# Optimization experiments

Measured on AMD Instinct MI355X. Metric: run time of the kernel, lower is better.

Reference implementation:

```python
import jax, jax.numpy as jnp
import numpy as np
from jax import lax

B, H, W, C = 8, 96, 96, 256
N_HEADS = 8
HEAD_DIM = C // N_HEADS
KS = 5  # depthwise LePE kernel


def setup_inputs() -> dict:
    key = jax.random.key(0)
    ks = jax.random.split(key, 12)
    s = 0.05  # xavier-ish scale for weights
    return {
        "x": jax.random.normal(ks[0], (B, H, W, C), jnp.float32),
        "encoder_layer": jax.random.normal(ks[1], (B, H, W, C), jnp.float32),
        "Wq": jax.random.normal(ks[2], (C, C), jnp.float32) * s,
        "bq": jnp.zeros((C,), jnp.float32),
        "Wk": jax.random.normal(ks[3], (C, C), jnp.float32) * s,
        "bk": jnp.zeros((C,), jnp.float32),
        "Wv": jax.random.normal(ks[4], (C, C), jnp.float32) * s,
        "bv": jnp.zeros((C,), jnp.float32),
        "conv_w": jax.random.normal(ks[5], (KS, KS, 1, C), jnp.float32) * s,  # HWIO depthwise
        "conv_b": jnp.zeros((C,), jnp.float32),
        "Wo": jax.random.normal(ks[6], (C, C), jnp.float32) * s,
        "bo": jnp.zeros((C,), jnp.float32),
        "rel_pos": jnp.zeros((1,), jnp.int32),  # unused by the module
    }


def _dwconv(v, conv_w, conv_b):
    # depthwise 5x5, stride 1, pad 2, NHWC
    y = lax.conv_general_dilated(
        v, conv_w, window_strides=(1, 1), padding=((2, 2), (2, 2)),
        dimension_numbers=("NHWC", "HWIO", "NHWC"), feature_group_count=v.shape[-1])
    return y + conv_b


def reference(x, encoder_layer, Wq, bq, Wk, bk, Wv, bv, conv_w, conv_b, Wo, bo, rel_pos):
    b, h, w, c = x.shape
    n, d = N_HEADS, c // N_HEADS
    scaling = jnp.asarray(d, x.dtype) ** -0.5

    q = x @ Wq + bq
    k = x @ Wk + bk + encoder_layer  # embed_dim != 64 branch
    v = x @ Wv + bv + encoder_layer

    lepe = _dwconv(v, conv_w, conv_b)  # (b,h,w,c)
    k = k * scaling

    qr = q.reshape(b, h, w, n, d)
    kr = k.reshape(b, h, w, n, d)
    vr = v.reshape(b, h, w, n, d)

    # width-wise axial attention: scores (b,h,n,w,w), LOG-softmax over keys
    A_w = jax.nn.log_softmax(jnp.einsum("bhind,bhjnd->bhnij", qr, kr), axis=-1)
    v1 = jnp.einsum("bhnij,bhjnd->bhind", A_w, vr)  # (b,h,w,n,d)

    # height-wise axial attention: scores (b,w,n,h,h), LOG-softmax over keys
    A_h = jax.nn.log_softmax(jnp.einsum("biwnd,bjwnd->bwnij", qr, kr), axis=-1)
    out = jnp.einsum("bwnij,bjwnd->biwnd", A_h, v1)  # (b,h,w,n,d)

    out = out.reshape(b, h, w, c) + lepe
    return out @ Wo + bo
```

## Files before the change

kernel.cpp:

```cpp
#include <hip/hip_runtime.h>

#define B_ 8
#define S_ 96
#define C_ 256
#define NH_ 8
#define D_ 32
#define M_ (B_*S_*S_)
static const size_t SZ = (size_t)M_ * C_;

typedef unsigned short u16;
typedef short bf16x8 __attribute__((ext_vector_type(8)));
typedef _Float16 hf8 __attribute__((ext_vector_type(8)));
typedef float f32x4 __attribute__((ext_vector_type(4)));

__device__ __forceinline__ u16 f2b(float f) {
    unsigned u = __float_as_uint(f);
    return (u16)((u + 0x7FFFu + ((u >> 16) & 1u)) >> 16);
}
__device__ __forceinline__ float b2f(u16 h) { return __uint_as_float(((unsigned)h) << 16); }
__device__ __forceinline__ u16 f2h(float f) {
    _Float16 h = (_Float16)f;
    return __builtin_bit_cast(u16, h);
}

__device__ __forceinline__ void gload16(const u16* g, u16* l) {
    __builtin_amdgcn_global_load_lds(
        (const __attribute__((address_space(1))) u16*)g,
        (__attribute__((address_space(3))) u16*)l, 16, 0, 0);
}

__global__ __launch_bounds__(256) void prep_x(
    const float* __restrict__ x, u16* __restrict__ xb)
{
    size_t base = ((size_t)blockIdx.x * 256 + threadIdx.x) * 8;
    float4 a = *(const float4*)(x + base);
    float4 b = *(const float4*)(x + base + 4);
    u16 o[8] = { f2b(a.x), f2b(a.y), f2b(a.z), f2b(a.w),
                 f2b(b.x), f2b(b.y), f2b(b.z), f2b(b.w) };
    *(int4*)(xb + base) = *(int4*)o;
}

__global__ __launch_bounds__(256) void prep_w(
    const float* __restrict__ Wq, const float* __restrict__ Wk,
    const float* __restrict__ Wv, const float* __restrict__ Wo,
    u16* __restrict__ WT)
{
    int id = blockIdx.x * 256 + threadIdx.x;
    int w = id >> 16;
    int r = id & 65535;
    int n = r >> 8;
    int kk = r & 255;
    const float* Wp = (w == 0) ? Wq : (w == 1) ? Wk : (w == 2) ? Wv : Wo;
    WT[(size_t)id] = f2b(Wp[(size_t)kk * 256 + n]);
}

__global__ __launch_bounds__(256) void prep_cw(
    const float* __restrict__ cw, u16* __restrict__ cwh)
{
    int id = blockIdx.x * 256 + threadIdx.x;
    cwh[id] = f2h(cw[id]);
}

#define STG(lds, gbase, k0)                                                     \
    _Pragma("unroll")                                                           \
    for (int i_ = 0; i_ < 2; ++i_) {                                            \
        int r16 = wave * 32 + i_ * 16;                                          \
        gload16((gbase) + (size_t)(r16 + srow) * C_ + (k0) + sslot * 8,         \
                (lds) + r16 * 32);                                              \
    }
#define FRAG(lds, cur, rowi) \
    (*(const bf16x8*)((lds) + (cur) * 4096 + (rowi) * 32 + (kg ^ (((rowi) >> 1) & 3)) * 8))

__global__ __launch_bounds__(256, 3) void proj_q(
    const u16* __restrict__ xb, const u16* __restrict__ WT,
    const float* __restrict__ bq, u16* __restrict__ q)
{
    __shared__ u16 sA[3 * 4096];
    __shared__ u16 sB[3 * 4096];
    const int t = threadIdx.x;
    const int colbase = blockIdx.x * 128;
    const int m0 = blockIdx.y * 128;
    const int wave = t >> 6, lane = t & 63;
    const int wr = wave >> 1, wc = wave & 1;
    const int l16 = lane & 15, kg = lane >> 4;
    const int srow = lane >> 2;
    const int sslot = (lane & 3) ^ ((lane >> 3) & 3);

    const u16* gA = xb + (size_t)m0 * C_;
    const u16* gB = WT + (size_t)colbase * C_;

    f32x4 acc[4][4];
#pragma unroll
    for (int i = 0; i < 4; ++i)
#pragma unroll
        for (int j = 0; j < 4; ++j) acc[i][j] = (f32x4){0.f, 0.f, 0.f, 0.f};

    STG(sA, gA, 0); STG(sB, gB, 0);
    STG(sA + 4096, gA, 32); STG(sB + 4096, gB, 32);
#pragma unroll
    for (int it = 0; it < 8; ++it) {
        const int cur = it % 3;
        if (it < 7) asm volatile("s_waitcnt vmcnt(4)" ::: "memory");
        else        asm volatile("s_waitcnt vmcnt(0)" ::: "memory");
        __builtin_amdgcn_s_barrier();
        __builtin_amdgcn_sched_barrier(0);
        if (it < 6) { STG(sA + ((it + 2) % 3) * 4096, gA, (it + 2) * 32);
                      STG(sB + ((it + 2) % 3) * 4096, gB, (it + 2) * 32); }
        bf16x8 af[4], bf[4];
#pragma unroll
        for (int mi = 0; mi < 4; ++mi)
            af[mi] = FRAG(sA, cur, wr * 64 + mi * 16 + l16);
#pragma unroll
        for (int ni = 0; ni < 4; ++ni)
            bf[ni] = FRAG(sB, cur, wc * 64 + ni * 16 + l16);
#pragma unroll
        for (int mi = 0; mi < 4; ++mi)
#pragma unroll
            for (int ni = 0; ni < 4; ++ni)
                acc[mi][ni] = __builtin_amdgcn_mfma_f32_16x16x32_bf16(
                    af[mi], bf[ni], acc[mi][ni], 0, 0, 0);
    }

#pragma unroll
    for (int mi = 0; mi < 4; ++mi)
#pragma unroll
        for (int ni = 0; ni < 4; ++ni) {
            int col = colbase + wc * 64 + ni * 16 + l16;
            float bqv = bq[col];
#pragma unroll
            for (int r = 0; r < 4; ++r) {
                int row = m0 + wr * 64 + mi * 16 + kg * 4 + r;
                q[(size_t)row * 256 + col] = f2b(acc[mi][ni][r] + bqv);
            }
        }
}

__global__ __launch_bounds__(256, 2) void proj_kv(
    const u16* __restrict__ xb, const float* __restrict__ enc,
    const u16* __restrict__ WT,
    const float* __restrict__ bk, const float* __restrict__ bv,
    u16* __restrict__ k, u16* __restrict__ v)
{
    __shared__ u16 sA[3 * 4096];
    __shared__ u16 sB0[3 * 4096];
    __shared__ u16 sB1[3 * 4096];
    const int t = threadIdx.x;
    const int colbase = blockIdx.x * 128;
    const int m0 = blockIdx.y * 128;
    const int wave = t >> 6, lane = t & 63;
    const int wr = wave >> 1, wc = wave & 1;
    const int l16 = lane & 15, kg = lane >> 4;
    const int srow = lane >> 2;
    const int sslot = (lane & 3) ^ ((lane >> 3) & 3);

    const u16* gA = xb + (size_t)m0 * C_;
    const u16* gB0 = WT + 65536 + (size_t)colbase * C_;
    const u16* gB1 = WT + 2 * 65536 + (size_t)colbase * C_;

    f32x4 acck[4][4], accv[4][4];
#pragma unroll
    for (int i = 0; i < 4; ++i)
#pragma unroll
        for (int j = 0; j < 4; ++j) {
            acck[i][j] = (f32x4){0.f, 0.f, 0.f, 0.f};
            accv[i][j] = (f32x4){0.f, 0.f, 0.f, 0.f};
        }

    STG(sA, gA, 0); STG(sB0, gB0, 0); STG(sB1, gB1, 0);
    STG(sA + 4096, gA, 32); STG(sB0 + 4096, gB0, 32); STG(sB1 + 4096, gB1, 32);
#pragma unroll
    for (int it = 0; it < 8; ++it) {
        const int cur = it % 3;
        if (it < 7) asm volatile("s_waitcnt vmcnt(6)" ::: "memory");
        else        asm volatile("s_waitcnt vmcnt(0)" ::: "memory");
        __builtin_amdgcn_s_barrier();
        __builtin_amdgcn_sched_barrier(0);
        if (it < 6) {
            int nb = ((it + 2) % 3) * 4096;
            STG(sA + nb, gA, (it + 2) * 32);
            STG(sB0 + nb, gB0, (it + 2) * 32);
            STG(sB1 + nb, gB1, (it + 2) * 32);
        }
        bf16x8 af[4], b0[4], b1[4];
#pragma unroll
        for (int mi = 0; mi < 4; ++mi)
            af[mi] = FRAG(sA, cur, wr * 64 + mi * 16 + l16);
#pragma unroll
        for (int ni = 0; ni < 4; ++ni) {
            b0[ni] = FRAG(sB0, cur, wc * 64 + ni * 16 + l16);
            b1[ni] = FRAG(sB1, cur, wc * 64 + ni * 16 + l16);
        }
#pragma unroll
        for (int mi = 0; mi < 4; ++mi)
#pragma unroll
            for (int ni = 0; ni < 4; ++ni) {
                acck[mi][ni] = __builtin_amdgcn_mfma_f32_16x16x32_bf16(
                    af[mi], b0[ni], acck[mi][ni], 0, 0, 0);
                accv[mi][ni] = __builtin_amdgcn_mfma_f32_16x16x32_bf16(
                    af[mi], b1[ni], accv[mi][ni], 0, 0, 0);
            }
    }

    const float SCALE = 0.17677669529663687f;
#pragma unroll
    for (int mi = 0; mi < 4; ++mi)
#pragma unroll
        for (int ni = 0; ni < 4; ++ni) {
            int col = colbase + wc * 64 + ni * 16 + l16;
            float bkv = bk[col], bvv = bv[col];
#pragma unroll
            for (int r = 0; r < 4; ++r) {
                int row = m0 + wr * 64 + mi * 16 + kg * 4 + r;
                size_t off = (size_t)row * 256 + col;
                float e = enc[off];
                k[off] = f2b((acck[mi][ni][r] + bkv + e) * SCALE);
                v[off] = f2h(accv[mi][ni][r] + bvv + e);
            }
        }
}

__global__ __launch_bounds__(256) void dwconv5x5(
    const u16* __restrict__ vh, const u16* __restrict__ cwh,
    const float* __restrict__ cb, u16* __restrict__ lepeb)
{
    size_t tid = (size_t)blockIdx.x * 256 + threadIdx.x;
    int c8 = (int)(tid & 31);
    size_t rest = tid >> 5;
    int wi = (int)(rest % 12);
    size_t tmp = rest / 12;
    int h = (int)(tmp % S_);
    int b = (int)(tmp / S_);
    int w0 = wi * 8;
    int c0 = c8 * 8;

    hf8 z;
#pragma unroll
    for (int q = 0; q < 8; ++q) z[q] = (_Float16)0.f;
    hf8 acc[8] = { z, z, z, z, z, z, z, z };

#pragma unroll
    for (int dy = -2; dy <= 2; ++dy) {
        int hy = h + dy;
        if (hy < 0 || hy >= S_) continue;
        const u16* rowp = vh + (((size_t)b * S_ + hy) * S_) * C_ + c0;
        hf8 vr[12];
#pragma unroll
        for (int i = 0; i < 12; ++i) {
            int c = w0 - 2 + i;
            vr[i] = (c >= 0 && c < S_) ? *(const hf8*)(rowp + (size_t)c * C_) : z;
        }
#pragma unroll
        for (int dx = 0; dx < 5; ++dx) {
            hf8 ww = *(const hf8*)(cwh + (size_t)((dy + 2) * 5 + dx) * C_ + c0);
#pragma unroll
            for (int r = 0; r < 8; ++r) acc[r] += vr[dx + r] * ww;
        }
    }

    float4 cb0 = *(const float4*)(cb + c0);
    float4 cb1 = *(const float4*)(cb + c0 + 4);
    float cbv[8] = { cb0.x, cb0.y, cb0.z, cb0.w, cb1.x, cb1.y, cb1.z, cb1.w };
    size_t pix0 = ((size_t)b * S_ + h) * S_ + w0;
#pragma unroll
    for (int r = 0; r < 8; ++r) {
        u16 o[8];
#pragma unroll
        for (int q = 0; q < 8; ++q) o[q] = f2b((float)acc[r][q] + cbv[q]);
        *(int4*)(lepeb + (pix0 + r) * C_ + c0) = *(int4*)o;
    }
}

template<int HM>
__global__ __launch_bounds__(128, 3) void axial(
    const u16* __restrict__ qb, const u16* __restrict__ kb,
    const void* __restrict__ vin, void* __restrict__ vout,
    const u16* __restrict__ lep, int ofac, int pstride)
{
    __shared__ u16 sQ[96][56];
    __shared__ u16 sK[96][56];
    __shared__ u16 sVT[HM + 1][32][104];
    __shared__ u16 sAh[2][16][40];
    __shared__ u16 sAl[2][16][40];

    const int t = threadIdx.x;
    const int wave = t >> 6, lane = t & 63;
    const int l16 = lane & 15, kg = lane >> 4;

    const int n = blockIdx.x & 7;
    const int o = (blockIdx.x >> 3) % 96;
    const int b = blockIdx.x / (8 * 96);
    const size_t base = ((size_t)b * 9216 + (size_t)o * ofac) * C_ + n * D_;

    if (t < 96) {
        const u16* gq = qb + base + (size_t)t * pstride;
        const u16* gk = kb + base + (size_t)t * pstride;
#pragma unroll
        for (int c = 0; c < 4; ++c) {
            *(int4*)&sQ[t][c * 8] = *(const int4*)(gq + c * 8);
            *(int4*)&sK[t][c * 8] = *(const int4*)(gk + c * 8);
        }
    }
    if (HM == 0) {
        const u16* vb = (const u16*)vin;
#pragma unroll
        for (int p = 0; p < 3; ++p) {
            int j = p * 32 + (t >> 2);
            int dc = (t & 3) * 8;
            int4 raw = *(const int4*)(vb + base + (size_t)j * pstride + dc);
            const u16* e = (const u16*)&raw;
#pragma unroll
            for (int q = 0; q < 8; ++q) sVT[0][dc + q][j] = e[q];
        }
    } else {
        const float* v1 = (const float*)vin;
#pragma unroll
        for (int p = 0; p < 6; ++p) {
            int j = p * 16 + (t >> 3);
            int db = (t & 7) * 4;
            float4 f = *(const float4*)(v1 + base + (size_t)j * pstride + db);
            float fv[4] = { f.x, f.y, f.z, f.w };
#pragma unroll
            for (int q = 0; q < 4; ++q) {
                u16 hi = f2b(fv[q]);
                sVT[0][db + q][j] = hi;
                sVT[HM][db + q][j] = f2b(fv[q] - b2f(hi));
            }
        }
    }
    __syncthreads();

    bf16x8 kf[6];
#pragma unroll
    for (int f = 0; f < 6; ++f)
        kf[f] = *(const bf16x8*)&sK[f * 16 + l16][kg * 8];

    const f32x4 zero = {0.f, 0.f, 0.f, 0.f};

    for (int p = 0; p < 3; ++p) {
        const int g = wave * 3 + p;
        bf16x8 qf = *(const bf16x8*)&sQ[g * 16 + l16][kg * 8];
        f32x4 s[6];
#pragma unroll
        for (int f = 0; f < 6; ++f)
            s[f] = __builtin_amdgcn_mfma_f32_16x16x32_bf16(kf[f], qf, zero, 0, 0, 0);

        float m = s[0][0];
#pragma unroll
        for (int f = 0; f < 6; ++f)
#pragma unroll
            for (int r = 0; r < 4; ++r) m = fmaxf(m, s[f][r]);
        m = fmaxf(m, __shfl_xor(m, 16));
        m = fmaxf(m, __shfl_xor(m, 32));
        float l = 0.f;
#pragma unroll
        for (int f = 0; f < 6; ++f)
#pragma unroll
            for (int r = 0; r < 4; ++r) l += __expf(s[f][r] - m);
        l += __shfl_xor(l, 16);
        l += __shfl_xor(l, 32);
        float lse = m + __logf(l);

        u16 ah[6][4], al[6][4];
#pragma unroll
        for (int f = 0; f < 6; ++f)
#pragma unroll
            for (int r = 0; r < 4; ++r) {
                float a = s[f][r] - lse;
                ah[f][r] = (HM == 0) ? f2h(a) : f2b(a);
                if (HM) al[f][r] = f2b(a - b2f(ah[f][r]));
            }

        f32x4 pacc[2] = { zero, zero };
#pragma unroll
        for (int c = 0; c < 3; ++c) {
#pragma unroll
            for (int fi = 0; fi < 2; ++fi)
#pragma unroll
                for (int r = 0; r < 4; ++r) {
                    int col = fi * 16 + kg * 4 + r;
                    sAh[wave][l16][col] = ah[2 * c + fi][r];
                    if (HM) sAl[wave][l16][col] = al[2 * c + fi][r];
                }
            if (HM == 0) {
                hf8 ahf = *(const hf8*)&sAh[wave][l16][kg * 8];
#pragma unroll
                for (int nf = 0; nf < 2; ++nf) {
                    hf8 vt = *(const hf8*)&sVT[0][nf * 16 + l16][c * 32 + kg * 8];
                    pacc[nf] = __builtin_amdgcn_mfma_f32_16x16x32_f16(ahf, vt, pacc[nf], 0, 0, 0);
                }
            } else {
                bf16x8 ahf = *(const bf16x8*)&sAh[wave][l16][kg * 8];
                bf16x8 alf = *(const bf16x8*)&sAl[wave][l16][kg * 8];
#pragma unroll
                for (int nf = 0; nf < 2; ++nf) {
                    bf16x8 vt = *(const bf16x8*)&sVT[0][nf * 16 + l16][c * 32 + kg * 8];
                    bf16x8 vtl = *(const bf16x8*)&sVT[HM][nf * 16 + l16][c * 32 + kg * 8];
                    pacc[nf] = __builtin_amdgcn_mfma_f32_16x16x32_bf16(ahf, vt, pacc[nf], 0, 0, 0);
                    pacc[nf] = __builtin_amdgcn_mfma_f32_16x16x32_bf16(ahf, vtl, pacc[nf], 0, 0, 0);
                    pacc[nf] = __builtin_amdgcn_mfma_f32_16x16x32_bf16(alf, vt, pacc[nf], 0, 0, 0);
                }
            }
        }

#pragma unroll
        for (int nf = 0; nf < 2; ++nf)
#pragma unroll
            for (int r = 0; r < 4; ++r) {
                int qi = g * 16 + kg * 4 + r;
                size_t off = base + (size_t)qi * pstride + nf * 16 + l16;
                if (HM == 0) {
                    ((float*)vout)[off] = pacc[nf][r];
                } else {
                    float lv = b2f(lep[off]);
                    ((u16*)vout)[off] = f2b(pacc[nf][r] + lv);
                }
            }
    }
}

__global__ __launch_bounds__(256, 3) void out_gemm(
    const u16* __restrict__ o2b, const u16* __restrict__ WoT,
    const float* __restrict__ bo, float* __restrict__ out)
{
    __shared__ u16 sA[3 * 4096];
    __shared__ u16 sB[3 * 4096];
    const int t = threadIdx.x;
    const int colbase = blockIdx.x * 128;
    const int m0 = blockIdx.y * 128;
    const int wave = t >> 6, lane = t & 63;
    const int wr = wave >> 1, wc = wave & 1;
    const int l16 = lane & 15, kg = lane >> 4;
    const int srow = lane >> 2;
    const int sslot = (lane & 3) ^ ((lane >> 3) & 3);

    const u16* gA = o2b + (size_t)m0 * C_;
    const u16* gB = WoT + (size_t)colbase * C_;

    f32x4 acc[4][4];
#pragma unroll
    for (int i = 0; i < 4; ++i)
#pragma unroll
        for (int j = 0; j < 4; ++j) acc[i][j] = (f32x4){0.f, 0.f, 0.f, 0.f};

    STG(sA, gA, 0); STG(sB, gB, 0);
    STG(sA + 4096, gA, 32); STG(sB + 4096, gB, 32);
#pragma unroll
    for (int it = 0; it < 8; ++it) {
        const int cur = it % 3;
        if (it < 7) asm volatile("s_waitcnt vmcnt(4)" ::: "memory");
        else        asm volatile("s_waitcnt vmcnt(0)" ::: "memory");
        __builtin_amdgcn_s_barrier();
        __builtin_amdgcn_sched_barrier(0);
        if (it < 6) { STG(sA + ((it + 2) % 3) * 4096, gA, (it + 2) * 32);
                      STG(sB + ((it + 2) % 3) * 4096, gB, (it + 2) * 32); }
        bf16x8 af[4], bf[4];
#pragma unroll
        for (int mi = 0; mi < 4; ++mi)
            af[mi] = FRAG(sA, cur, wr * 64 + mi * 16 + l16);
#pragma unroll
        for (int ni = 0; ni < 4; ++ni)
            bf[ni] = FRAG(sB, cur, wc * 64 + ni * 16 + l16);
#pragma unroll
        for (int mi = 0; mi < 4; ++mi)
#pragma unroll
            for (int ni = 0; ni < 4; ++ni)
                acc[mi][ni] = __builtin_amdgcn_mfma_f32_16x16x32_bf16(
                    af[mi], bf[ni], acc[mi][ni], 0, 0, 0);
    }

#pragma unroll
    for (int mi = 0; mi < 4; ++mi)
#pragma unroll
        for (int ni = 0; ni < 4; ++ni) {
            int col = colbase + wc * 64 + ni * 16 + l16;
            float bv_ = bo[col];
#pragma unroll
            for (int r = 0; r < 4; ++r) {
                int row = m0 + wr * 64 + mi * 16 + kg * 4 + r;
                out[(size_t)row * 256 + col] = acc[mi][ni][r] + bv_;
            }
        }
}

extern "C" void kernel_launch(void* const* d_in, const int* in_sizes, int n_in,
                              void* d_out, int out_size, void* d_ws, size_t ws_size,
                              hipStream_t stream)
{
    const float* x   = (const float*)d_in[0];
    const float* enc = (const float*)d_in[1];
    const float* Wq  = (const float*)d_in[2];
    const float* bq  = (const float*)d_in[3];
    const float* Wk  = (const float*)d_in[4];
    const float* bk  = (const float*)d_in[5];
    const float* Wv  = (const float*)d_in[6];
    const float* bv  = (const float*)d_in[7];
    const float* cw  = (const float*)d_in[8];
    const float* cb  = (const float*)d_in[9];
    const float* Wo  = (const float*)d_in[10];
    const float* bo  = (const float*)d_in[11];

    u16* qbuf = (u16*)d_ws;
    u16* kbuf = qbuf + SZ;
    u16* vbuf = kbuf + SZ;
    u16* WT   = vbuf + SZ;
    u16* cwh  = WT + 4 * 65536;
    u16* xb   = cwh + 6400;
    u16* lep  = xb + SZ;
    float* v1 = (float*)d_out;

    prep_x<<<9216, 256, 0, stream>>>(x, xb);
    prep_w<<<1024, 256, 0, stream>>>(Wq, Wk, Wv, Wo, WT);
    prep_cw<<<25, 256, 0, stream>>>(cw, cwh);
    proj_q<<<dim3(2, 576), 256, 0, stream>>>(xb, WT, bq, qbuf);
    proj_kv<<<dim3(2, 576), 256, 0, stream>>>(xb, enc, WT, bk, bv, kbuf, vbuf);
    dwconv5x5<<<1152, 256, 0, stream>>>(vbuf, cwh, cb, lep);
    axial<0><<<B_ * 96 * NH_, 128, 0, stream>>>(qbuf, kbuf, vbuf, v1, nullptr, 96, 256);
    axial<1><<<B_ * 96 * NH_, 128, 0, stream>>>(qbuf, kbuf, v1, qbuf, lep, 1, 96 * 256);
    out_gemm<<<dim3(2, 576), 256, 0, stream>>>(qbuf, WT + 3 * 65536, bo, (float*)d_out);
}
```

Measured before the change: 291.5 us.

## Stage GEMM epilogues through LDS for vector stores; store v1 as fp16

The three GEMM kernels now transpose their accumulators through a swizzled shared-memory buffer, one half-tile at a time. Each thread then writes contiguous 16-byte vectors of q/k/v/out, with bias and encoder loads vectorised as well; previously each thread issued scattered 2- or 4-byte stores. Separately, the intermediate v1 between the two axial passes is stored as fp16 instead of fp32, and the second pass uses a single fp16 MFMA instead of the three-product bf16 hi/lo split. This cuts intermediate traffic and matrix work but lowers the precision of the height-wise attention, since log-softmax values can be large in magnitude.

```diff
diff --git a/kernel.cpp b/kernel.cpp
--- a/kernel.cpp
+++ b/kernel.cpp
@@ -71,12 +71,27 @@
 #define FRAG(lds, cur, rowi) \
     (*(const bf16x8*)((lds) + (cur) * 4096 + (rowi) * 32 + (kg ^ (((rowi) >> 1) & 3)) * 8))
 
+#define TPUT(sT, accs)                                                          \
+    _Pragma("unroll")                                                           \
+    for (int mi = 0; mi < 4; ++mi)                                              \
+    _Pragma("unroll")                                                           \
+        for (int ni = 0; ni < 4; ++ni) {                                        \
+            int colq = wc * 16 + ni * 4 + (l16 >> 2);                           \
+            _Pragma("unroll")                                                   \
+            for (int r = 0; r < 4; ++r) {                                       \
+                int row = mi * 16 + kg * 4 + r;                                 \
+                (sT)[row * 128 + ((colq ^ (row & 31)) << 2) + (l16 & 3)] =      \
+                    accs[mi][ni][r];                                            \
+            }                                                                   \
+        }
+
 __global__ __launch_bounds__(256, 3) void proj_q(
     const u16* __restrict__ xb, const u16* __restrict__ WT,
     const float* __restrict__ bq, u16* __restrict__ q)
 {
-    __shared__ u16 sA[3 * 4096];
-    __shared__ u16 sB[3 * 4096];
+    __shared__ u16 smem[24576];
+    u16* sA = smem;
+    u16* sB = smem + 12288;
     const int t = threadIdx.x;
     const int colbase = blockIdx.x * 128;
     const int m0 = blockIdx.y * 128;
@@ -121,18 +136,30 @@
                     af[mi], bf[ni], acc[mi][ni], 0, 0, 0);
     }
 
-#pragma unroll
-    for (int mi = 0; mi < 4; ++mi)
-#pragma unroll
-        for (int ni = 0; ni < 4; ++ni) {
-            int col = colbase + wc * 64 + ni * 16 + l16;
-            float bqv = bq[col];
-#pragma unroll
-            for (int r = 0; r < 4; ++r) {
-                int row = m0 + wr * 64 + mi * 16 + kg * 4 + r;
-                q[(size_t)row * 256 + col] = f2b(acc[mi][ni][r] + bqv);
-            }
-        }
+    float* sT = (float*)smem;
+    const int erow = t >> 2, cg = t & 3;
+    __syncthreads();
+#pragma unroll
+    for (int half = 0; half < 2; ++half) {
+        if (half) __syncthreads();
+        if (wr == half) { TPUT(sT, acc); }
+        __syncthreads();
+        int grow = m0 + half * 64 + erow;
+        u16 outv[32];
+#pragma unroll
+        for (int i = 0; i < 8; ++i) {
+            int cql = cg * 8 + i;
+            float4 vv = *(float4*)&sT[erow * 128 + ((cql ^ (erow & 31)) << 2)];
+            float4 bb = *(const float4*)(bq + colbase + cql * 4);
+            outv[i * 4 + 0] = f2b(vv.x + bb.x);
+            outv[i * 4 + 1] = f2b(vv.y + bb.y);
+            outv[i * 4 + 2] = f2b(vv.z + bb.z);
+            outv[i * 4 + 3] = f2b(vv.w + bb.w);
+        }
+        u16* dst = q + (size_t)grow * 256 + colbase + cg * 32;
+#pragma unroll
+        for (int s = 0; s < 4; ++s) *(int4*)(dst + s * 8) = *(int4*)(outv + s * 8);
+    }
 }
 
 __global__ __launch_bounds__(256, 2) void proj_kv(
@@ -141,9 +168,10 @@
     const float* __restrict__ bk, const float* __restrict__ bv,
     u16* __restrict__ k, u16* __restrict__ v)
 {
-    __shared__ u16 sA[3 * 4096];
-    __shared__ u16 sB0[3 * 4096];
-    __shared__ u16 sB1[3 * 4096];
+    __shared__ u16 smem[36864];
+    u16* sA  = smem;
+    u16* sB0 = smem + 12288;
+    u16* sB1 = smem + 24576;
     const int t = threadIdx.x;
     const int colbase = blockIdx.x * 128;
     const int m0 = blockIdx.y * 128;
@@ -202,21 +230,44 @@
     }
 
     const float SCALE = 0.17677669529663687f;
-#pragma unroll
-    for (int mi = 0; mi < 4; ++mi)
-#pragma unroll
-        for (int ni = 0; ni < 4; ++ni) {
-            int col = colbase + wc * 64 + ni * 16 + l16;
-            float bkv = bk[col], bvv = bv[col];
-#pragma unroll
-            for (int r = 0; r < 4; ++r) {
-                int row = m0 + wr * 64 + mi * 16 + kg * 4 + r;
-                size_t off = (size_t)row * 256 + col;
-                float e = enc[off];
-                k[off] = f2b((acck[mi][ni][r] + bkv + e) * SCALE);
-                v[off] = f2h(accv[mi][ni][r] + bvv + e);
-            }
-        }
+    float* sTk = (float*)smem;
+    float* sTv = (float*)smem + 8192;
+    const int erow = t >> 2, cg = t & 3;
+    __syncthreads();
+#pragma unroll
+    for (int half = 0; half < 2; ++half) {
+        if (half) __syncthreads();
+        if (wr == half) { TPUT(sTk, acck); TPUT(sTv, accv); }
+        __syncthreads();
+        int grow = m0 + half * 64 + erow;
+        const float* ep = enc + (size_t)grow * 256 + colbase + cg * 32;
+        u16 ko[32], vo[32];
+#pragma unroll
+        for (int i = 0; i < 8; ++i) {
+            int cql = cg * 8 + i;
+            int soff = erow * 128 + ((cql ^ (erow & 31)) << 2);
+            float4 kv = *(float4*)&sTk[soff];
+            float4 vv = *(float4*)&sTv[soff];
+            float4 ee = *(const float4*)(ep + i * 4);
+            float4 kb = *(const float4*)(bk + colbase + cql * 4);
+            float4 vb_ = *(const float4*)(bv + colbase + cql * 4);
+            ko[i * 4 + 0] = f2b((kv.x + kb.x + ee.x) * SCALE);
+            ko[i * 4 + 1] = f2b((kv.y + kb.y + ee.y) * SCALE);
+            ko[i * 4 + 2] = f2b((kv.z + kb.z + ee.z) * SCALE);
+            ko[i * 4 + 3] = f2b((kv.w + kb.w + ee.w) * SCALE);
+            vo[i * 4 + 0] = f2h(vv.x + vb_.x + ee.x);
+            vo[i * 4 + 1] = f2h(vv.y + vb_.y + ee.y);
+            vo[i * 4 + 2] = f2h(vv.z + vb_.z + ee.z);
+            vo[i * 4 + 3] = f2h(vv.w + vb_.w + ee.w);
+        }
+        u16* kd = k + (size_t)grow * 256 + colbase + cg * 32;
+        u16* vd = v + (size_t)grow * 256 + colbase + cg * 32;
+#pragma unroll
+        for (int s = 0; s < 4; ++s) {
+            *(int4*)(kd + s * 8) = *(int4*)(ko + s * 8);
+            *(int4*)(vd + s * 8) = *(int4*)(vo + s * 8);
+        }
+    }
 }
 
 __global__ __launch_bounds__(256) void dwconv5x5(
@@ -273,14 +324,13 @@
 template<int HM>
 __global__ __launch_bounds__(128, 3) void axial(
     const u16* __restrict__ qb, const u16* __restrict__ kb,
-    const void* __restrict__ vin, void* __restrict__ vout,
+    const u16* __restrict__ vin, void* __restrict__ vout,
     const u16* __restrict__ lep, int ofac, int pstride)
 {
     __shared__ u16 sQ[96][56];
     __shared__ u16 sK[96][56];
-    __shared__ u16 sVT[HM + 1][32][104];
+    __shared__ u16 sVT[32][104];
     __shared__ u16 sAh[2][16][40];
-    __shared__ u16 sAl[2][16][40];
 
     const int t = threadIdx.x;
     const int wave = t >> 6, lane = t & 63;
@@ -300,32 +350,14 @@
             *(int4*)&sK[t][c * 8] = *(const int4*)(gk + c * 8);
         }
     }
-    if (HM == 0) {
-        const u16* vb = (const u16*)vin;
-#pragma unroll
-        for (int p = 0; p < 3; ++p) {
-            int j = p * 32 + (t >> 2);
-            int dc = (t & 3) * 8;
-            int4 raw = *(const int4*)(vb + base + (size_t)j * pstride + dc);
-            const u16* e = (const u16*)&raw;
-#pragma unroll
-            for (int q = 0; q < 8; ++q) sVT[0][dc + q][j] = e[q];
-        }
-    } else {
-        const float* v1 = (const float*)vin;
-#pragma unroll
-        for (int p = 0; p < 6; ++p) {
-            int j = p * 16 + (t >> 3);
-            int db = (t & 7) * 4;
-            float4 f = *(const float4*)(v1 + base + (size_t)j * pstride + db);
-            float fv[4] = { f.x, f.y, f.z, f.w };
-#pragma unroll
-            for (int q = 0; q < 4; ++q) {
-                u16 hi = f2b(fv[q]);
-                sVT[0][db + q][j] = hi;
-                sVT[HM][db + q][j] = f2b(fv[q] - b2f(hi));
-            }
-        }
+#pragma unroll
+    for (int p = 0; p < 3; ++p) {
+        int j = p * 32 + (t >> 2);
+        int dc = (t & 3) * 8;
+        int4 raw = *(const int4*)(vin + base + (size_t)j * pstride + dc);
+        const u16* e = (const u16*)&raw;
+#pragma unroll
+        for (int q = 0; q < 8; ++q) sVT[dc + q][j] = e[q];
     }
     __syncthreads();
 
@@ -360,15 +392,12 @@
         l += __shfl_xor(l, 32);
         float lse = m + __logf(l);
 
-        u16 ah[6][4], al[6][4];
+        u16 ah[6][4];
 #pragma unroll
         for (int f = 0; f < 6; ++f)
 #pragma unroll
-            for (int r = 0; r < 4; ++r) {
-                float a = s[f][r] - lse;
-                ah[f][r] = (HM == 0) ? f2h(a) : f2b(a);
-                if (HM) al[f][r] = f2b(a - b2f(ah[f][r]));
-            }
+            for (int r = 0; r < 4; ++r)
+                ah[f][r] = f2h(s[f][r] - lse);
 
         f32x4 pacc[2] = { zero, zero };
 #pragma unroll
@@ -376,29 +405,13 @@
 #pragma unroll
             for (int fi = 0; fi < 2; ++fi)
 #pragma unroll
-                for (int r = 0; r < 4; ++r) {
-                    int col = fi * 16 + kg * 4 + r;
-                    sAh[wave][l16][col] = ah[2 * c + fi][r];
-                    if (HM) sAl[wave][l16][col] = al[2 * c + fi][r];
-                }
-            if (HM == 0) {
-                hf8 ahf = *(const hf8*)&sAh[wave][l16][kg * 8];
-#pragma unroll
-                for (int nf = 0; nf < 2; ++nf) {
-                    hf8 vt = *(const hf8*)&sVT[0][nf * 16 + l16][c * 32 + kg * 8];
-                    pacc[nf] = __builtin_amdgcn_mfma_f32_16x16x32_f16(ahf, vt, pacc[nf], 0, 0, 0);
-                }
-            } else {
-                bf16x8 ahf = *(const bf16x8*)&sAh[wave][l16][kg * 8];
-                bf16x8 alf = *(const bf16x8*)&sAl[wave][l16][kg * 8];
-#pragma unroll
-                for (int nf = 0; nf < 2; ++nf) {
-                    bf16x8 vt = *(const bf16x8*)&sVT[0][nf * 16 + l16][c * 32 + kg * 8];
-                    bf16x8 vtl = *(const bf16x8*)&sVT[HM][nf * 16 + l16][c * 32 + kg * 8];
-                    pacc[nf] = __builtin_amdgcn_mfma_f32_16x16x32_bf16(ahf, vt, pacc[nf], 0, 0, 0);
-                    pacc[nf] = __builtin_amdgcn_mfma_f32_16x16x32_bf16(ahf, vtl, pacc[nf], 0, 0, 0);
-                    pacc[nf] = __builtin_amdgcn_mfma_f32_16x16x32_bf16(alf, vt, pacc[nf], 0, 0, 0);
-                }
+                for (int r = 0; r < 4; ++r)
+                    sAh[wave][l16][fi * 16 + kg * 4 + r] = ah[2 * c + fi][r];
+            hf8 ahf = *(const hf8*)&sAh[wave][l16][kg * 8];
+#pragma unroll
+            for (int nf = 0; nf < 2; ++nf) {
+                hf8 vt = *(const hf8*)&sVT[nf * 16 + l16][c * 32 + kg * 8];
+                pacc[nf] = __builtin_amdgcn_mfma_f32_16x16x32_f16(ahf, vt, pacc[nf], 0, 0, 0);
             }
         }
 
@@ -409,7 +422,7 @@
                 int qi = g * 16 + kg * 4 + r;
                 size_t off = base + (size_t)qi * pstride + nf * 16 + l16;
                 if (HM == 0) {
-                    ((float*)vout)[off] = pacc[nf][r];
+                    ((u16*)vout)[off] = f2h(pacc[nf][r]);
                 } else {
                     float lv = b2f(lep[off]);
                     ((u16*)vout)[off] = f2b(pacc[nf][r] + lv);
@@ -422,8 +435,9 @@
     const u16* __restrict__ o2b, const u16* __restrict__ WoT,
     const float* __restrict__ bo, float* __restrict__ out)
 {
-    __shared__ u16 sA[3 * 4096];
-    __shared__ u16 sB[3 * 4096];
+    __shared__ u16 smem[24576];
+    u16* sA = smem;
+    u16* sB = smem + 12288;
     const int t = threadIdx.x;
     const int colbase = blockIdx.x * 128;
     const int m0 = blockIdx.y * 128;
@@ -468,18 +482,25 @@
                     af[mi], bf[ni], acc[mi][ni], 0, 0, 0);
     }
 
-#pragma unroll
-    for (int mi = 0; mi < 4; ++mi)
-#pragma unroll
-        for (int ni = 0; ni < 4; ++ni) {
-            int col = colbase + wc * 64 + ni * 16 + l16;
-            float bv_ = bo[col];
-#pragma unroll
-            for (int r = 0; r < 4; ++r) {
-                int row = m0 + wr * 64 + mi * 16 + kg * 4 + r;
-                out[(size_t)row * 256 + col] = acc[mi][ni][r] + bv_;
-            }
-        }
+    float* sT = (float*)smem;
+    const int erow = t >> 2, cg = t & 3;
+    __syncthreads();
+#pragma unroll
+    for (int half = 0; half < 2; ++half) {
+        if (half) __syncthreads();
+        if (wr == half) { TPUT(sT, acc); }
+        __syncthreads();
+        int grow = m0 + half * 64 + erow;
+        float* dst = out + (size_t)grow * 256 + colbase + cg * 32;
+#pragma unroll
+        for (int i = 0; i < 8; ++i) {
+            int cql = cg * 8 + i;
+            float4 vv = *(float4*)&sT[erow * 128 + ((cql ^ (erow & 31)) << 2)];
+            float4 bb = *(const float4*)(bo + colbase + cql * 4);
+            float4 res = { vv.x + bb.x, vv.y + bb.y, vv.z + bb.z, vv.w + bb.w };
+            *(float4*)(dst + i * 4) = res;
+        }
+    }
 }
 
 extern "C" void kernel_launch(void* const* d_in, const int* in_sizes, int n_in,
@@ -506,7 +527,7 @@
     u16* cwh  = WT + 4 * 65536;
     u16* xb   = cwh + 6400;
     u16* lep  = xb + SZ;
-    float* v1 = (float*)d_out;
+    u16* v1h  = (u16*)d_out;
 
     prep_x<<<9216, 256, 0, stream>>>(x, xb);
     prep_w<<<1024, 256, 0, stream>>>(Wq, Wk, Wv, Wo, WT);
@@ -514,7 +535,7 @@
     proj_q<<<dim3(2, 576), 256, 0, stream>>>(xb, WT, bq, qbuf);
     proj_kv<<<dim3(2, 576), 256, 0, stream>>>(xb, enc, WT, bk, bv, kbuf, vbuf);
     dwconv5x5<<<1152, 256, 0, stream>>>(vbuf, cwh, cb, lep);
-    axial<0><<<B_ * 96 * NH_, 128, 0, stream>>>(qbuf, kbuf, vbuf, v1, nullptr, 96, 256);
-    axial<1><<<B_ * 96 * NH_, 128, 0, stream>>>(qbuf, kbuf, v1, qbuf, lep, 1, 96 * 256);
+    axial<0><<<B_ * 96 * NH_, 128, 0, stream>>>(qbuf, kbuf, vbuf, v1h, nullptr, 96, 256);
+    axial<1><<<B_ * 96 * NH_, 128, 0, stream>>>(qbuf, kbuf, v1h, qbuf, lep, 1, 96 * 256);
     out_gemm<<<dim3(2, 576), 256, 0, stream>>>(qbuf, WT + 3 * 65536, bo, (float*)d_out);
 }
```

New measurement: 303.7 us. +4.2%, slower.
